# Kernel optimization log

Measured on AMD Instinct MI355X. Metric: run time of the kernel, lower is better.

Reference implementation:

```python
import jax, jax.numpy as jnp
import numpy as np

T, B, D, H = 512, 64, 1024, 1024


def _lstm_layer(x, W_ih, W_hh, b):
    """x: [T,B,in] -> (out [T,B,H], h_n [B,H], c_n [B,H]). Gate order i,f,g,o."""
    xW = jnp.einsum('tbi,ij->tbj', x, W_ih) + b  # precompute input projections [T,B,4H]
    Bsz = x.shape[1]
    Hsz = W_hh.shape[0]
    h0 = jnp.zeros((Bsz, Hsz), dtype=x.dtype)

    def step(carry, xw_t):
        h, c = carry
        gates = xw_t + h @ W_hh  # [B,4H]
        i, f, g, o = jnp.split(gates, 4, axis=-1)
        i = jax.nn.sigmoid(i)
        f = jax.nn.sigmoid(f)
        g = jnp.tanh(g)
        o = jax.nn.sigmoid(o)
        c_next = f * c + i * g
        h_next = o * jnp.tanh(c_next)
        return (h_next, c_next), h_next

    (h_n, c_n), out = jax.lax.scan(step, (h0, h0), xW)
    return out, h_n, c_n


def setup_inputs() -> dict:
    key = jax.random.key(0)
    ks = jax.random.split(key, 7)
    s_in = 1.0 / np.sqrt(H)
    return {
        'x': jax.random.normal(ks[0], (T, B, D), dtype=jnp.float32),
        'W_ih0': jax.random.normal(ks[1], (D, 4 * H), dtype=jnp.float32) * s_in,
        'W_hh0': jax.random.normal(ks[2], (H, 4 * H), dtype=jnp.float32) * s_in,
        'b0': jax.random.normal(ks[3], (4 * H,), dtype=jnp.float32) * s_in,
        'W_ih1': jax.random.normal(ks[4], (H, 4 * H), dtype=jnp.float32) * s_in,
        'W_hh1': jax.random.normal(ks[5], (H, 4 * H), dtype=jnp.float32) * s_in,
        'b1': jax.random.normal(ks[6], (4 * H,), dtype=jnp.float32) * s_in,
    }


def reference(x, W_ih0, W_hh0, b0, W_ih1, W_hh1, b1):
    # layer 0
    out0, h0n, c0n = _lstm_layer(x, W_ih0, W_hh0, b0)
    # dropout=0 -> identity between layers
    out1, h1n, c1n = _lstm_layer(out0, W_ih1, W_hh1, b1)
    h_n = jnp.stack([h0n, h1n], 0)  # [L,B,H]
    c_n = jnp.stack([c0n, c1n], 0)
    return out1, (h_n, c_n)
```

## Files before the change

kernel.cpp:

```cpp
#include <hip/hip_runtime.h>
#include <hip/hip_bf16.h>

#define TSTEPS 512
#define NSTEPS 256
#define BATCH  64
#define HDIM   1024
#define NROWS  (TSTEPS*BATCH)

typedef __attribute__((ext_vector_type(8))) short bf16x8;
typedef __attribute__((ext_vector_type(4))) float f32x4;

__device__ __forceinline__ unsigned short f2bf(float f){
    unsigned u = __float_as_uint(f);
    u += 0x7fffu + ((u >> 16) & 1u);
    return (unsigned short)(u >> 16);
}
__device__ __forceinline__ float bf2f(unsigned short s){
    return __uint_as_float(((unsigned)s) << 16);
}

__device__ __forceinline__ void gridbar(unsigned int* region, unsigned int epoch){
    unsigned int* slots = region;
    unsigned int* rel   = region + 8192;
    __syncthreads();
    if (blockIdx.x == 0){
        const int i = threadIdx.x;
        if (i > 0 && i < 256){
            while (__hip_atomic_load(&slots[i*32], __ATOMIC_RELAXED, __HIP_MEMORY_SCOPE_AGENT) < epoch)
                __builtin_amdgcn_s_sleep(2);
        }
        __syncthreads();
        if (i < 256){
            unsigned int old = __hip_atomic_exchange(&rel[i*32], epoch,
                                   __ATOMIC_RELAXED, __HIP_MEMORY_SCOPE_AGENT);
            asm volatile("" :: "v"(old));
        }
    } else {
        if (threadIdx.x == 0){
            unsigned int old = __hip_atomic_exchange(&slots[blockIdx.x*32], epoch,
                                   __ATOMIC_RELAXED, __HIP_MEMORY_SCOPE_AGENT);
            asm volatile("" :: "v"(old));
            while (__hip_atomic_load(&rel[blockIdx.x*32], __ATOMIC_RELAXED, __HIP_MEMORY_SCOPE_AGENT) < epoch)
                __builtin_amdgcn_s_sleep(2);
        }
        __syncthreads();
    }
    asm volatile("" ::: "memory");
}

__global__ __launch_bounds__(256)
void split_transpose_w(const float* __restrict__ W,
                       unsigned short* __restrict__ WThi,
                       unsigned short* __restrict__ WTlo)
{
    __shared__ float tile[32][33];
    const int c0 = blockIdx.x * 32;
    const int k0 = blockIdx.y * 32;
    const int tx = threadIdx.x & 31, ty = threadIdx.x >> 5;
    #pragma unroll
    for (int r=0;r<4;++r)
        tile[ty + r*8][tx] = W[(size_t)(k0 + ty + r*8)*4096 + c0 + tx];
    __syncthreads();
    #pragma unroll
    for (int r=0;r<4;++r){
        float v = tile[tx][ty + r*8];
        unsigned short hi = f2bf(v);
        unsigned short lo = f2bf(v - bf2f(hi));
        WThi[(size_t)(c0 + ty + r*8)*1024 + k0 + tx] = hi;
        WTlo[(size_t)(c0 + ty + r*8)*1024 + k0 + tx] = lo;
    }
}

__global__ __launch_bounds__(256)
void reorder_whh_t(const float* __restrict__ W,
                   unsigned short* __restrict__ Whi,
                   unsigned short* __restrict__ Wlo)
{
    const int bid = blockIdx.x;
    const int j  = threadIdx.x & 15;
    const int k0 = threadIdx.x >> 4;
    const int col = (j>>2)*1024 + bid*4 + (j&3);
    for (int k = k0; k < 1024; k += 16){
        float v = W[(size_t)k*4096 + col];
        unsigned short hi = f2bf(v);
        unsigned short lo = f2bf(v - bf2f(hi));
        Whi[((size_t)bid*16 + j)*1024 + k] = hi;
        Wlo[((size_t)bid*16 + j)*1024 + k] = lo;
    }
}

__global__ __launch_bounds__(256)
void gemm_xw_split(const float* __restrict__ A,
                   const unsigned short* __restrict__ BThi,
                   const unsigned short* __restrict__ BTlo,
                   const float* __restrict__ bias, unsigned short* __restrict__ gp)
{
    __shared__ __align__(16) unsigned short Ahi[128*32];
    __shared__ __align__(16) unsigned short Alo[128*32];
    __shared__ __align__(16) unsigned short Bhi[128*32];
    __shared__ __align__(16) unsigned short Blo[128*32];

    const int tid = threadIdx.x;
    const int w = tid >> 6, l = tid & 63;
    const int bx = blockIdx.x & 31, by = blockIdx.x >> 5;
    const int row0 = by*128, col0 = bx*128;
    const int wrow = (w>>1)*64, wcol = (w&1)*64;

    const int srow  = l >> 2;
    const int skoff = (l & 3) * 8;

    const int arow  = tid >> 1;
    const int akoff = (tid & 1) * 16;
    const float* aptr = A + (size_t)(row0 + arow)*1024 + akoff;

    f32x4 acc[4][4];
    #pragma unroll
    for (int m=0;m<4;++m)
        #pragma unroll
        for (int n=0;n<4;++n)
            acc[m][n] = (f32x4){0.f,0.f,0.f,0.f};

    for (int k0=0; k0<1024; k0+=32){
        #pragma unroll
        for (int c=0;c<2;++c){
            const int i = w*2 + c;
            const unsigned short* gh = BThi + (size_t)(col0 + i*16 + srow)*1024 + k0 + skoff;
            const unsigned short* gl = BTlo + (size_t)(col0 + i*16 + srow)*1024 + k0 + skoff;
            __builtin_amdgcn_global_load_lds((const __attribute__((address_space(1))) void*)gh,
                (__attribute__((address_space(3))) void*)(Bhi + i*512), 16, 0, 0);
            __builtin_amdgcn_global_load_lds((const __attribute__((address_space(1))) void*)gl,
                (__attribute__((address_space(3))) void*)(Blo + i*512), 16, 0, 0);
        }
        {
            float4 x0 = *reinterpret_cast<const float4*>(aptr + k0);
            float4 x1 = *reinterpret_cast<const float4*>(aptr + k0 + 4);
            float4 x2 = *reinterpret_cast<const float4*>(aptr + k0 + 8);
            float4 x3 = *reinterpret_cast<const float4*>(aptr + k0 + 12);
            float xs[16] = {x0.x,x0.y,x0.z,x0.w, x1.x,x1.y,x1.z,x1.w,
                            x2.x,x2.y,x2.z,x2.w, x3.x,x3.y,x3.z,x3.w};
            unsigned short hs[16], ls[16];
            #pragma unroll
            for (int e=0;e<16;++e){
                hs[e] = f2bf(xs[e]);
                ls[e] = f2bf(xs[e] - bf2f(hs[e]));
            }
            #pragma unroll
            for (int q=0;q<4;++q){
                ushort4 h4; h4.x=hs[q*4]; h4.y=hs[q*4+1]; h4.z=hs[q*4+2]; h4.w=hs[q*4+3];
                ushort4 l4; l4.x=ls[q*4]; l4.y=ls[q*4+1]; l4.z=ls[q*4+2]; l4.w=ls[q*4+3];
                *reinterpret_cast<ushort4*>(&Ahi[arow*32 + akoff + q*4]) = h4;
                *reinterpret_cast<ushort4*>(&Alo[arow*32 + akoff + q*4]) = l4;
            }
        }
        __syncthreads();
        bf16x8 afh[4], afl[4], bfh[4], bfl[4];
        #pragma unroll
        for (int m=0;m<4;++m){
            const int off = (wrow + m*16 + (l&15))*32 + (l>>4)*8;
            afh[m] = *reinterpret_cast<const bf16x8*>(&Ahi[off]);
            afl[m] = *reinterpret_cast<const bf16x8*>(&Alo[off]);
        }
        #pragma unroll
        for (int n=0;n<4;++n){
            const int off = (wcol + n*16 + (l&15))*32 + (l>>4)*8;
            bfh[n] = *reinterpret_cast<const bf16x8*>(&Bhi[off]);
            bfl[n] = *reinterpret_cast<const bf16x8*>(&Blo[off]);
        }
        #pragma unroll
        for (int m=0;m<4;++m)
            #pragma unroll
            for (int n=0;n<4;++n){
                acc[m][n] = __builtin_amdgcn_mfma_f32_16x16x32_bf16(afh[m], bfh[n], acc[m][n], 0,0,0);
                acc[m][n] = __builtin_amdgcn_mfma_f32_16x16x32_bf16(afl[m], bfh[n], acc[m][n], 0,0,0);
                acc[m][n] = __builtin_amdgcn_mfma_f32_16x16x32_bf16(afh[m], bfl[n], acc[m][n], 0,0,0);
            }
        __syncthreads();
    }

    #pragma unroll
    for (int n=0;n<4;++n){
        const int n_g = col0 + wcol + n*16 + (l&15);
        const float bv = bias[n_g];
        const int g = n_g >> 10, hcol = n_g & 1023;
        const int bid = hcol >> 2, hj = hcol & 3;
        #pragma unroll
        for (int m=0;m<4;++m){
            #pragma unroll
            for (int r=0;r<4;++r){
                const int m_g = row0 + wrow + m*16 + (l>>4)*4 + r;
                const int t = m_g >> 6, b = m_g & 63;
                gp[(((size_t)t*256 + bid)*64 + b)*16 + g*4 + hj] = f2bf(acc[m][n][r] + bv);
            }
        }
    }
}

__global__ __launch_bounds__(512)
void lstm_mfma(const unsigned short* __restrict__ gp,
               const unsigned short* __restrict__ Whi,
               const unsigned short* __restrict__ Wlo,
               float* __restrict__ out,
               unsigned short* __restrict__ rhi, unsigned short* __restrict__ rlo,
               float* __restrict__ ctg, float* __restrict__ hn, float* __restrict__ cn,
               unsigned int* __restrict__ bar, int first, int last)
{
    __shared__ float pacc[8][64*17];
    __shared__ float xwlds[64*17];
    __shared__ float hout[256];

    const int tid  = threadIdx.x;
    const int bidx = blockIdx.x;
    const int w = tid >> 6, l = tid & 63;
    const int kbase = w << 7;

    bf16x8 wfh[4], wfl[4];
    {
        const unsigned short* bh = Whi + ((size_t)bidx*16 + (l&15))*1024 + kbase + (l>>4)*8;
        const unsigned short* bl = Wlo + ((size_t)bidx*16 + (l&15))*1024 + kbase + (l>>4)*8;
        #pragma unroll
        for (int ks=0; ks<4; ++ks){
            wfh[ks] = *reinterpret_cast<const bf16x8*>(bh + ks*32);
            wfl[ks] = *reinterpret_cast<const bf16x8*>(bl + ks*32);
        }
    }

    float creg = 0.f;
    if (!first && tid < 256) creg = ctg[bidx*256 + tid];
    if (first && tid < 64){
        unsigned long long o1 = __hip_atomic_exchange(
            reinterpret_cast<unsigned long long*>(rhi + (size_t)256*65536 + tid*1024 + bidx*4),
            0ull, __ATOMIC_RELAXED, __HIP_MEMORY_SCOPE_AGENT);
        unsigned long long o2 = __hip_atomic_exchange(
            reinterpret_cast<unsigned long long*>(rlo + (size_t)256*65536 + tid*1024 + bidx*4),
            0ull, __ATOMIC_RELAXED, __HIP_MEMORY_SCOPE_AGENT);
        asm volatile("" :: "v"(o1), "v"(o2));
    }
    gridbar(bar, 1);

    const int bq = tid & 63;
    const int hc = tid >> 6;

    for (int t=0; t<NSTEPS; ++t){
        if (tid < 128){
            bf16x8 v = *reinterpret_cast<const bf16x8*>(
                gp + (size_t)t*262144 + (size_t)bidx*1024 + tid*8);
            const int b = tid >> 1, j0 = (tid & 1)*8;
            float* xp = &xwlds[b*17 + j0];
            #pragma unroll
            for (int e=0;e<8;++e) xp[e] = bf2f((unsigned short)v[e]);
        }

        const int rs = (t > 0) ? (t-1) : (first ? 256 : NSTEPS-1);
        const unsigned short* hbh = rhi + (size_t)rs*65536 + kbase + (l>>4)*8;
        const unsigned short* hbl = rlo + (size_t)rs*65536 + kbase + (l>>4)*8;

        f32x4 acc[4];
        #pragma unroll
        for (int mt=0; mt<4; ++mt) acc[mt] = (f32x4){0.f,0.f,0.f,0.f};

        #pragma unroll
        for (int mt=0; mt<4; ++mt){
            const size_t row = (size_t)(mt*16 + (l&15)) * 1024;
            #pragma unroll
            for (int ks=0; ks<4; ++ks){
                bf16x8 ah = *reinterpret_cast<const bf16x8*>(hbh + row + ks*32);
                bf16x8 al = *reinterpret_cast<const bf16x8*>(hbl + row + ks*32);
                acc[mt] = __builtin_amdgcn_mfma_f32_16x16x32_bf16(ah, wfh[ks], acc[mt], 0,0,0);
                acc[mt] = __builtin_amdgcn_mfma_f32_16x16x32_bf16(al, wfh[ks], acc[mt], 0,0,0);
                acc[mt] = __builtin_amdgcn_mfma_f32_16x16x32_bf16(ah, wfl[ks], acc[mt], 0,0,0);
            }
        }
        #pragma unroll
        for (int mt=0; mt<4; ++mt){
            #pragma unroll
            for (int r=0; r<4; ++r){
                const int m = mt*16 + (l>>4)*4 + r;
                pacc[w][m*17 + (l&15)] = acc[mt][r];
            }
        }
        __syncthreads();

        if (tid < 256){
            float gs[4];
            #pragma unroll
            for (int g=0; g<4; ++g){
                const int idx = bq*17 + g*4 + hc;
                float s = xwlds[idx];
                #pragma unroll
                for (int pw=0; pw<8; ++pw) s += pacc[pw][idx];
                gs[g] = s;
            }
            float ig = 1.f/(1.f + __expf(-gs[0]));
            float fg = 1.f/(1.f + __expf(-gs[1]));
            float gg = tanhf(gs[2]);
            float og = 1.f/(1.f + __expf(-gs[3]));
            float c_new = fg * creg + ig * gg;
            float h_new = og * tanhf(c_new);
            creg = c_new;
            hout[bq*4 + hc] = h_new;
            if (last && t == NSTEPS-1){
                const int hcolg = bidx*4 + hc;
                hn[(size_t)bq*1024 + hcolg] = h_new;
                cn[(size_t)bq*1024 + hcolg] = c_new;
            }
        }
        __syncthreads();

        if (tid < 64){
            const int b = tid;
            float h0 = hout[b*4+0], h1 = hout[b*4+1], h2 = hout[b*4+2], h3 = hout[b*4+3];
            unsigned short p0 = f2bf(h0), p1 = f2bf(h1), p2 = f2bf(h2), p3 = f2bf(h3);
            unsigned short q0 = f2bf(h0 - bf2f(p0)), q1 = f2bf(h1 - bf2f(p1));
            unsigned short q2 = f2bf(h2 - bf2f(p2)), q3 = f2bf(h3 - bf2f(p3));
            unsigned long long phi = (unsigned long long)p0 | ((unsigned long long)p1<<16)
                                   | ((unsigned long long)p2<<32) | ((unsigned long long)p3<<48);
            unsigned long long plo = (unsigned long long)q0 | ((unsigned long long)q1<<16)
                                   | ((unsigned long long)q2<<32) | ((unsigned long long)q3<<48);
            unsigned long long o1 = __hip_atomic_exchange(
                reinterpret_cast<unsigned long long*>(rhi + (size_t)t*65536 + b*1024 + bidx*4),
                phi, __ATOMIC_RELAXED, __HIP_MEMORY_SCOPE_AGENT);
            unsigned long long o2 = __hip_atomic_exchange(
                reinterpret_cast<unsigned long long*>(rlo + (size_t)t*65536 + b*1024 + bidx*4),
                plo, __ATOMIC_RELAXED, __HIP_MEMORY_SCOPE_AGENT);
            asm volatile("" :: "v"(o1), "v"(o2));
            *reinterpret_cast<float4*>(&out[(size_t)t*65536 + (size_t)b*1024 + bidx*4]) =
                make_float4(h0, h1, h2, h3);
        }
        gridbar(bar, t + 2);
    }
    if (tid < 256) ctg[bidx*256 + tid] = creg;
}

extern "C" void kernel_launch(void* const* d_in, const int* in_sizes, int n_in,
                              void* d_out, int out_size, void* d_ws, size_t ws_size,
                              hipStream_t stream)
{
    const float* x    = (const float*)d_in[0];
    const float* Wih0 = (const float*)d_in[1];
    const float* Whh0 = (const float*)d_in[2];
    const float* b0   = (const float*)d_in[3];
    const float* Wih1 = (const float*)d_in[4];
    const float* Whh1 = (const float*)d_in[5];
    const float* b1   = (const float*)d_in[6];

    float* out1 = (float*)d_out;
    float* hn   = out1 + (size_t)NROWS*HDIM;
    float* cn   = hn + 2*BATCH*HDIM;

    float* out0 = out1;

    char* wsb = (char*)d_ws;
    unsigned short* gp    = (unsigned short*)wsb;
    unsigned short* WThi0 = (unsigned short*)(wsb + 134217728ull);
    unsigned short* WTlo0 = (unsigned short*)(wsb + 142606336ull);
    unsigned short* WThi1 = (unsigned short*)(wsb + 150994944ull);
    unsigned short* WTlo1 = (unsigned short*)(wsb + 159383552ull);
    unsigned short* Wthi0 = (unsigned short*)(wsb + 167772160ull);
    unsigned short* Wtlo0 = (unsigned short*)(wsb + 176160768ull);
    unsigned short* Wthi1 = (unsigned short*)(wsb + 184549376ull);
    unsigned short* Wtlo1 = (unsigned short*)(wsb + 192937984ull);
    unsigned short* rhi   = (unsigned short*)(wsb + 201326592ull);
    unsigned short* rlo   = (unsigned short*)(wsb + 235012096ull);
    float*          ctg   = (float*)(wsb + 268697600ull);
    unsigned int*   bar   = (unsigned int*)(wsb + 268959744ull);

    hipMemsetAsync(bar, 0, 262144, stream);
    split_transpose_w<<<dim3(128,32),256,0,stream>>>(Wih0, WThi0, WTlo0);
    split_transpose_w<<<dim3(128,32),256,0,stream>>>(Wih1, WThi1, WTlo1);
    reorder_whh_t<<<256,256,0,stream>>>(Whh0, Wthi0, Wtlo0);
    reorder_whh_t<<<256,256,0,stream>>>(Whh1, Wthi1, Wtlo1);

    const float*          Ain [2] = {x, out0};
    const unsigned short* Whi [2] = {WThi0, WThi1};
    const unsigned short* Wlo [2] = {WTlo0, WTlo1};
    const float*          bia [2] = {b0, b1};
    const unsigned short* wth [2] = {Wthi0, Wthi1};
    const unsigned short* wtl [2] = {Wtlo0, Wtlo1};
    float*                outp[2] = {out0, out1};

    for (int layer=0; layer<2; ++layer){
        float* hnL = hn + (size_t)layer*BATCH*HDIM;
        float* cnL = cn + (size_t)layer*BATCH*HDIM;
        for (int chunk=0; chunk<2; ++chunk){
            gemm_xw_split<<<4096,256,0,stream>>>(
                Ain[layer] + (size_t)chunk*NSTEPS*BATCH*HDIM,
                Whi[layer], Wlo[layer], bia[layer], gp);

            const unsigned short* gpc = gp;
            const unsigned short* wh = wth[layer];
            const unsigned short* wl = wtl[layer];
            float* op = outp[layer] + (size_t)chunk*NSTEPS*BATCH*HDIM;
            unsigned short* r1 = rhi; unsigned short* r2 = rlo;
            float* cg_ = ctg;
            unsigned int* br = bar + (size_t)(layer*2 + chunk)*16384;
            int first = (chunk == 0), last = (chunk == 1);
            void* args[12] = {(void*)&gpc, (void*)&wh, (void*)&wl, (void*)&op,
                              (void*)&r1, (void*)&r2, (void*)&cg_,
                              (void*)&hnL, (void*)&cnL,
                              (void*)&br, (void*)&first, (void*)&last};
            hipLaunchCooperativeKernel(reinterpret_cast<void*>(&lstm_mfma),
                                       dim3(256), dim3(512), args, 0, stream);
        }
    }
}
```

Measured before the change: 13.43 ms.

## Fuse both LSTM layers into one wavefront-pipelined cooperative kernel

Replaces the per-layer recurrent kernels with a single 1024-thread-per-block kernel. One half of each block runs layer 0 at step r while the other half runs layer 1 at step r-1. Layer 1's input projection is computed inside the recurrence from layer 0's freshly published hidden state, so the separate layer-1 input GEMM and the layer-0 output round-trip through global memory go away. The number of grid-wide barriers roughly halves. In exchange, each step doubles block size and register pressure, and the layer-1 half does twice the MFMA work per step. The time is split into four chunks of 128 steps for the layer-0 input projection buffer.

New measurement: 15.35 ms. 1.14x slower.

```diff
diff --git a/kernel.cpp b/kernel.cpp
--- a/kernel.cpp
+++ b/kernel.cpp
@@ -2,7 +2,7 @@
 #include <hip/hip_bf16.h>
 
 #define TSTEPS 512
-#define NSTEPS 256
+#define NSTEPS 128
 #define BATCH  64
 #define HDIM   1024
 #define NROWS  (TSTEPS*BATCH)
@@ -195,99 +195,151 @@
     }
 }
 
-__global__ __launch_bounds__(512)
-void lstm_mfma(const unsigned short* __restrict__ gp,
-               const unsigned short* __restrict__ Whi,
-               const unsigned short* __restrict__ Wlo,
-               float* __restrict__ out,
-               unsigned short* __restrict__ rhi, unsigned short* __restrict__ rlo,
-               float* __restrict__ ctg, float* __restrict__ hn, float* __restrict__ cn,
-               unsigned int* __restrict__ bar, int first, int last)
+__global__ __launch_bounds__(1024)
+void lstm_fused(const unsigned short* __restrict__ gp,
+                const unsigned short* __restrict__ Wh0h, const unsigned short* __restrict__ Wh0l,
+                const unsigned short* __restrict__ Wi1h, const unsigned short* __restrict__ Wi1l,
+                const unsigned short* __restrict__ Wh1h, const unsigned short* __restrict__ Wh1l,
+                const float* __restrict__ bias1, float* __restrict__ out1,
+                unsigned short* __restrict__ r0h, unsigned short* __restrict__ r0l,
+                unsigned short* __restrict__ r1h, unsigned short* __restrict__ r1l,
+                float* __restrict__ ctg, float* __restrict__ hn, float* __restrict__ cn,
+                unsigned int* __restrict__ bar, int first, int last)
 {
-    __shared__ float pacc[8][64*17];
+    __shared__ float pacc[2][8][64*17];
     __shared__ float xwlds[64*17];
-    __shared__ float hout[256];
+    __shared__ float hout[2][256];
 
     const int tid  = threadIdx.x;
+    const int vb   = tid >> 9;
+    const int vt   = tid & 511;
     const int bidx = blockIdx.x;
-    const int w = tid >> 6, l = tid & 63;
+    const int w = vt >> 6, l = vt & 63;
     const int kbase = w << 7;
-
-    bf16x8 wfh[4], wfl[4];
+    const int foff = kbase + (l>>4)*8;
+
+    bf16x8 wah[4], wal[4], wbh[4], wbl[4];
     {
-        const unsigned short* bh = Whi + ((size_t)bidx*16 + (l&15))*1024 + kbase + (l>>4)*8;
-        const unsigned short* bl = Wlo + ((size_t)bidx*16 + (l&15))*1024 + kbase + (l>>4)*8;
+        const size_t wo = ((size_t)bidx*16 + (l&15))*1024 + foff;
+        const unsigned short* pah = (vb==0 ? Wh0h : Wi1h) + wo;
+        const unsigned short* pal = (vb==0 ? Wh0l : Wi1l) + wo;
         #pragma unroll
         for (int ks=0; ks<4; ++ks){
-            wfh[ks] = *reinterpret_cast<const bf16x8*>(bh + ks*32);
-            wfl[ks] = *reinterpret_cast<const bf16x8*>(bl + ks*32);
-        }
+            wah[ks] = *reinterpret_cast<const bf16x8*>(pah + ks*32);
+            wal[ks] = *reinterpret_cast<const bf16x8*>(pal + ks*32);
+        }
+        if (vb == 1){
+            const unsigned short* pbh = Wh1h + wo;
+            const unsigned short* pbl = Wh1l + wo;
+            #pragma unroll
+            for (int ks=0; ks<4; ++ks){
+                wbh[ks] = *reinterpret_cast<const bf16x8*>(pbh + ks*32);
+                wbl[ks] = *reinterpret_cast<const bf16x8*>(pbl + ks*32);
+            }
+        }
+    }
+
+    float b1r[4] = {0.f,0.f,0.f,0.f};
+    if (vb == 1 && vt < 256){
+        const int col = bidx*4 + (vt>>6);
+        #pragma unroll
+        for (int g=0; g<4; ++g) b1r[g] = bias1[g*1024 + col];
     }
 
     float creg = 0.f;
-    if (!first && tid < 256) creg = ctg[bidx*256 + tid];
-    if (first && tid < 64){
+    if (!first && vt < 256) creg = ctg[vb*65536 + bidx*256 + vt];
+    if (first && vt < 64){
+        unsigned short* rh = (vb==0) ? r0h : r1h;
+        unsigned short* rl = (vb==0) ? r0l : r1l;
         unsigned long long o1 = __hip_atomic_exchange(
-            reinterpret_cast<unsigned long long*>(rhi + (size_t)256*65536 + tid*1024 + bidx*4),
+            reinterpret_cast<unsigned long long*>(rh + (size_t)NSTEPS*65536 + vt*1024 + bidx*4),
             0ull, __ATOMIC_RELAXED, __HIP_MEMORY_SCOPE_AGENT);
         unsigned long long o2 = __hip_atomic_exchange(
-            reinterpret_cast<unsigned long long*>(rlo + (size_t)256*65536 + tid*1024 + bidx*4),
+            reinterpret_cast<unsigned long long*>(rl + (size_t)NSTEPS*65536 + vt*1024 + bidx*4),
             0ull, __ATOMIC_RELAXED, __HIP_MEMORY_SCOPE_AGENT);
         asm volatile("" :: "v"(o1), "v"(o2));
     }
     gridbar(bar, 1);
 
-    const int bq = tid & 63;
-    const int hc = tid >> 6;
-
-    for (int t=0; t<NSTEPS; ++t){
-        if (tid < 128){
-            bf16x8 v = *reinterpret_cast<const bf16x8*>(
-                gp + (size_t)t*262144 + (size_t)bidx*1024 + tid*8);
-            const int b = tid >> 1, j0 = (tid & 1)*8;
-            float* xp = &xwlds[b*17 + j0];
-            #pragma unroll
-            for (int e=0;e<8;++e) xp[e] = bf2f((unsigned short)v[e]);
-        }
-
-        const int rs = (t > 0) ? (t-1) : (first ? 256 : NSTEPS-1);
-        const unsigned short* hbh = rhi + (size_t)rs*65536 + kbase + (l>>4)*8;
-        const unsigned short* hbl = rlo + (size_t)rs*65536 + kbase + (l>>4)*8;
-
-        f32x4 acc[4];
-        #pragma unroll
-        for (int mt=0; mt<4; ++mt) acc[mt] = (f32x4){0.f,0.f,0.f,0.f};
-
-        #pragma unroll
-        for (int mt=0; mt<4; ++mt){
-            const size_t row = (size_t)(mt*16 + (l&15)) * 1024;
-            #pragma unroll
-            for (int ks=0; ks<4; ++ks){
-                bf16x8 ah = *reinterpret_cast<const bf16x8*>(hbh + row + ks*32);
-                bf16x8 al = *reinterpret_cast<const bf16x8*>(hbl + row + ks*32);
-                acc[mt] = __builtin_amdgcn_mfma_f32_16x16x32_bf16(ah, wfh[ks], acc[mt], 0,0,0);
-                acc[mt] = __builtin_amdgcn_mfma_f32_16x16x32_bf16(al, wfh[ks], acc[mt], 0,0,0);
-                acc[mt] = __builtin_amdgcn_mfma_f32_16x16x32_bf16(ah, wfl[ks], acc[mt], 0,0,0);
-            }
-        }
-        #pragma unroll
-        for (int mt=0; mt<4; ++mt){
-            #pragma unroll
-            for (int r=0; r<4; ++r){
-                const int m = mt*16 + (l>>4)*4 + r;
-                pacc[w][m*17 + (l&15)] = acc[mt][r];
-            }
-        }
-        __syncthreads();
-
-        if (tid < 256){
+    const int bq = vt & 63;
+    const int hc = vt >> 6;
+
+    for (int r=0; r<=NSTEPS; ++r){
+        if (vb == 0 && r < NSTEPS){
+            if (vt < 128){
+                bf16x8 v = *reinterpret_cast<const bf16x8*>(
+                    gp + (size_t)r*262144 + (size_t)bidx*1024 + vt*8);
+                const int b = vt >> 1, j0 = (vt & 1)*8;
+                float* xp = &xwlds[b*17 + j0];
+                #pragma unroll
+                for (int e=0;e<8;++e) xp[e] = bf2f((unsigned short)v[e]);
+            }
+            const int rs0 = (r > 0) ? r-1 : (first ? NSTEPS : NSTEPS-1);
+            const unsigned short* hbh = r0h + (size_t)rs0*65536 + foff;
+            const unsigned short* hbl = r0l + (size_t)rs0*65536 + foff;
+            f32x4 acc[4];
+            #pragma unroll
+            for (int mt=0; mt<4; ++mt) acc[mt] = (f32x4){0.f,0.f,0.f,0.f};
+            #pragma unroll
+            for (int mt=0; mt<4; ++mt){
+                const size_t row = (size_t)(mt*16 + (l&15)) * 1024;
+                #pragma unroll
+                for (int ks=0; ks<4; ++ks){
+                    bf16x8 ah = *reinterpret_cast<const bf16x8*>(hbh + row + ks*32);
+                    bf16x8 al = *reinterpret_cast<const bf16x8*>(hbl + row + ks*32);
+                    acc[mt] = __builtin_amdgcn_mfma_f32_16x16x32_bf16(ah, wah[ks], acc[mt], 0,0,0);
+                    acc[mt] = __builtin_amdgcn_mfma_f32_16x16x32_bf16(al, wah[ks], acc[mt], 0,0,0);
+                    acc[mt] = __builtin_amdgcn_mfma_f32_16x16x32_bf16(ah, wal[ks], acc[mt], 0,0,0);
+                }
+            }
+            #pragma unroll
+            for (int mt=0; mt<4; ++mt)
+                #pragma unroll
+                for (int q=0; q<4; ++q)
+                    pacc[0][w][(mt*16 + (l>>4)*4 + q)*17 + (l&15)] = acc[mt][q];
+        } else if (vb == 1 && r >= 1){
+            const unsigned short* xbh = r0h + (size_t)(r-1)*65536 + foff;
+            const unsigned short* xbl = r0l + (size_t)(r-1)*65536 + foff;
+            const int rs1 = (r >= 2) ? r-2 : (first ? NSTEPS : NSTEPS-1);
+            const unsigned short* hbh = r1h + (size_t)rs1*65536 + foff;
+            const unsigned short* hbl = r1l + (size_t)rs1*65536 + foff;
+            f32x4 acc[4];
+            #pragma unroll
+            for (int mt=0; mt<4; ++mt) acc[mt] = (f32x4){0.f,0.f,0.f,0.f};
+            #pragma unroll
+            for (int mt=0; mt<4; ++mt){
+                const size_t row = (size_t)(mt*16 + (l&15)) * 1024;
+                #pragma unroll
+                for (int ks=0; ks<4; ++ks){
+                    bf16x8 xh = *reinterpret_cast<const bf16x8*>(xbh + row + ks*32);
+                    bf16x8 xl = *reinterpret_cast<const bf16x8*>(xbl + row + ks*32);
+                    acc[mt] = __builtin_amdgcn_mfma_f32_16x16x32_bf16(xh, wah[ks], acc[mt], 0,0,0);
+                    acc[mt] = __builtin_amdgcn_mfma_f32_16x16x32_bf16(xl, wah[ks], acc[mt], 0,0,0);
+                    acc[mt] = __builtin_amdgcn_mfma_f32_16x16x32_bf16(xh, wal[ks], acc[mt], 0,0,0);
+                    bf16x8 ah = *reinterpret_cast<const bf16x8*>(hbh + row + ks*32);
+                    bf16x8 al = *reinterpret_cast<const bf16x8*>(hbl + row + ks*32);
+                    acc[mt] = __builtin_amdgcn_mfma_f32_16x16x32_bf16(ah, wbh[ks], acc[mt], 0,0,0);
+                    acc[mt] = __builtin_amdgcn_mfma_f32_16x16x32_bf16(al, wbh[ks], acc[mt], 0,0,0);
+                    acc[mt] = __builtin_amdgcn_mfma_f32_16x16x32_bf16(ah, wbl[ks], acc[mt], 0,0,0);
+                }
+            }
+            #pragma unroll
+            for (int mt=0; mt<4; ++mt)
+                #pragma unroll
+                for (int q=0; q<4; ++q)
+                    pacc[1][w][(mt*16 + (l>>4)*4 + q)*17 + (l&15)] = acc[mt][q];
+        }
+        __syncthreads();
+
+        const bool act = (vb==0) ? (r < NSTEPS) : (r >= 1);
+        if (vt < 256 && act){
             float gs[4];
             #pragma unroll
             for (int g=0; g<4; ++g){
                 const int idx = bq*17 + g*4 + hc;
-                float s = xwlds[idx];
-                #pragma unroll
-                for (int pw=0; pw<8; ++pw) s += pacc[pw][idx];
+                float s = (vb==0) ? xwlds[idx] : b1r[g];
+                #pragma unroll
+                for (int pw=0; pw<8; ++pw) s += pacc[vb][pw][idx];
                 gs[g] = s;
             }
             float ig = 1.f/(1.f + __expf(-gs[0]));
@@ -297,38 +349,47 @@
             float c_new = fg * creg + ig * gg;
             float h_new = og * tanhf(c_new);
             creg = c_new;
-            hout[bq*4 + hc] = h_new;
-            if (last && t == NSTEPS-1){
-                const int hcolg = bidx*4 + hc;
+            hout[vb][bq*4 + hc] = h_new;
+            const int hcolg = bidx*4 + hc;
+            if (vb==0 && last && r == NSTEPS-1){
                 hn[(size_t)bq*1024 + hcolg] = h_new;
                 cn[(size_t)bq*1024 + hcolg] = c_new;
             }
-        }
-        __syncthreads();
-
-        if (tid < 64){
-            const int b = tid;
-            float h0 = hout[b*4+0], h1 = hout[b*4+1], h2 = hout[b*4+2], h3 = hout[b*4+3];
-            unsigned short p0 = f2bf(h0), p1 = f2bf(h1), p2 = f2bf(h2), p3 = f2bf(h3);
-            unsigned short q0 = f2bf(h0 - bf2f(p0)), q1 = f2bf(h1 - bf2f(p1));
-            unsigned short q2 = f2bf(h2 - bf2f(p2)), q3 = f2bf(h3 - bf2f(p3));
+            if (vb==1 && last && r == NSTEPS){
+                hn[65536 + (size_t)bq*1024 + hcolg] = h_new;
+                cn[65536 + (size_t)bq*1024 + hcolg] = c_new;
+            }
+        }
+        __syncthreads();
+
+        if (vt < 64 && act){
+            const int b = vt;
+            float h0v = hout[vb][b*4+0], h1v = hout[vb][b*4+1];
+            float h2v = hout[vb][b*4+2], h3v = hout[vb][b*4+3];
+            unsigned short p0 = f2bf(h0v), p1 = f2bf(h1v), p2 = f2bf(h2v), p3 = f2bf(h3v);
+            unsigned short q0 = f2bf(h0v - bf2f(p0)), q1 = f2bf(h1v - bf2f(p1));
+            unsigned short q2 = f2bf(h2v - bf2f(p2)), q3 = f2bf(h3v - bf2f(p3));
             unsigned long long phi = (unsigned long long)p0 | ((unsigned long long)p1<<16)
                                    | ((unsigned long long)p2<<32) | ((unsigned long long)p3<<48);
             unsigned long long plo = (unsigned long long)q0 | ((unsigned long long)q1<<16)
                                    | ((unsigned long long)q2<<32) | ((unsigned long long)q3<<48);
+            const int slot = (vb==0) ? r : r-1;
+            unsigned short* rh = (vb==0) ? r0h : r1h;
+            unsigned short* rl = (vb==0) ? r0l : r1l;
             unsigned long long o1 = __hip_atomic_exchange(
-                reinterpret_cast<unsigned long long*>(rhi + (size_t)t*65536 + b*1024 + bidx*4),
+                reinterpret_cast<unsigned long long*>(rh + (size_t)slot*65536 + b*1024 + bidx*4),
                 phi, __ATOMIC_RELAXED, __HIP_MEMORY_SCOPE_AGENT);
             unsigned long long o2 = __hip_atomic_exchange(
-                reinterpret_cast<unsigned long long*>(rlo + (size_t)t*65536 + b*1024 + bidx*4),
+                reinterpret_cast<unsigned long long*>(rl + (size_t)slot*65536 + b*1024 + bidx*4),
                 plo, __ATOMIC_RELAXED, __HIP_MEMORY_SCOPE_AGENT);
             asm volatile("" :: "v"(o1), "v"(o2));
-            *reinterpret_cast<float4*>(&out[(size_t)t*65536 + (size_t)b*1024 + bidx*4]) =
-                make_float4(h0, h1, h2, h3);
-        }
-        gridbar(bar, t + 2);
-    }
-    if (tid < 256) ctg[bidx*256 + tid] = creg;
+            if (vb == 1)
+                *reinterpret_cast<float4*>(&out1[(size_t)(r-1)*65536 + (size_t)b*1024 + bidx*4]) =
+                    make_float4(h0v, h1v, h2v, h3v);
+        }
+        gridbar(bar, r + 2);
+    }
+    if (vt < 256) ctg[vb*65536 + bidx*256 + vt] = creg;
 }
 
 extern "C" void kernel_launch(void* const* d_in, const int* in_sizes, int n_in,
@@ -347,59 +408,50 @@
     float* hn   = out1 + (size_t)NROWS*HDIM;
     float* cn   = hn + 2*BATCH*HDIM;
 
-    float* out0 = out1;
-
     char* wsb = (char*)d_ws;
     unsigned short* gp    = (unsigned short*)wsb;
-    unsigned short* WThi0 = (unsigned short*)(wsb + 134217728ull);
-    unsigned short* WTlo0 = (unsigned short*)(wsb + 142606336ull);
-    unsigned short* WThi1 = (unsigned short*)(wsb + 150994944ull);
-    unsigned short* WTlo1 = (unsigned short*)(wsb + 159383552ull);
-    unsigned short* Wthi0 = (unsigned short*)(wsb + 167772160ull);
-    unsigned short* Wtlo0 = (unsigned short*)(wsb + 176160768ull);
-    unsigned short* Wthi1 = (unsigned short*)(wsb + 184549376ull);
-    unsigned short* Wtlo1 = (unsigned short*)(wsb + 192937984ull);
-    unsigned short* rhi   = (unsigned short*)(wsb + 201326592ull);
-    unsigned short* rlo   = (unsigned short*)(wsb + 235012096ull);
-    float*          ctg   = (float*)(wsb + 268697600ull);
-    unsigned int*   bar   = (unsigned int*)(wsb + 268959744ull);
+    unsigned short* WThi0 = (unsigned short*)(wsb +  67108864ull);
+    unsigned short* WTlo0 = (unsigned short*)(wsb +  75497472ull);
+    unsigned short* Wh0h  = (unsigned short*)(wsb +  83886080ull);
+    unsigned short* Wh0l  = (unsigned short*)(wsb +  92274688ull);
+    unsigned short* Wi1h  = (unsigned short*)(wsb + 100663296ull);
+    unsigned short* Wi1l  = (unsigned short*)(wsb + 109051904ull);
+    unsigned short* Wh1h  = (unsigned short*)(wsb + 117440512ull);
+    unsigned short* Wh1l  = (unsigned short*)(wsb + 125829120ull);
+    unsigned short* r0h   = (unsigned short*)(wsb + 134217728ull);
+    unsigned short* r0l   = (unsigned short*)(wsb + 151126016ull);
+    unsigned short* r1h   = (unsigned short*)(wsb + 168034304ull);
+    unsigned short* r1l   = (unsigned short*)(wsb + 184942592ull);
+    float*          ctg   = (float*)(wsb + 201850880ull);
+    unsigned int*   bar   = (unsigned int*)(wsb + 202375168ull);
 
     hipMemsetAsync(bar, 0, 262144, stream);
     split_transpose_w<<<dim3(128,32),256,0,stream>>>(Wih0, WThi0, WTlo0);
-    split_transpose_w<<<dim3(128,32),256,0,stream>>>(Wih1, WThi1, WTlo1);
-    reorder_whh_t<<<256,256,0,stream>>>(Whh0, Wthi0, Wtlo0);
-    reorder_whh_t<<<256,256,0,stream>>>(Whh1, Wthi1, Wtlo1);
-
-    const float*          Ain [2] = {x, out0};
-    const unsigned short* Whi [2] = {WThi0, WThi1};
-    const unsigned short* Wlo [2] = {WTlo0, WTlo1};
-    const float*          bia [2] = {b0, b1};
-    const unsigned short* wth [2] = {Wthi0, Wthi1};
-    const unsigned short* wtl [2] = {Wtlo0, Wtlo1};
-    float*                outp[2] = {out0, out1};
-
-    for (int layer=0; layer<2; ++layer){
-        float* hnL = hn + (size_t)layer*BATCH*HDIM;
-        float* cnL = cn + (size_t)layer*BATCH*HDIM;
-        for (int chunk=0; chunk<2; ++chunk){
-            gemm_xw_split<<<4096,256,0,stream>>>(
-                Ain[layer] + (size_t)chunk*NSTEPS*BATCH*HDIM,
-                Whi[layer], Wlo[layer], bia[layer], gp);
-
-            const unsigned short* gpc = gp;
-            const unsigned short* wh = wth[layer];
-            const unsigned short* wl = wtl[layer];
-            float* op = outp[layer] + (size_t)chunk*NSTEPS*BATCH*HDIM;
-            unsigned short* r1 = rhi; unsigned short* r2 = rlo;
-            float* cg_ = ctg;
-            unsigned int* br = bar + (size_t)(layer*2 + chunk)*16384;
-            int first = (chunk == 0), last = (chunk == 1);
-            void* args[12] = {(void*)&gpc, (void*)&wh, (void*)&wl, (void*)&op,
-                              (void*)&r1, (void*)&r2, (void*)&cg_,
-                              (void*)&hnL, (void*)&cnL,
-                              (void*)&br, (void*)&first, (void*)&last};
-            hipLaunchCooperativeKernel(reinterpret_cast<void*>(&lstm_mfma),
-                                       dim3(256), dim3(512), args, 0, stream);
-        }
-    }
-}
+    reorder_whh_t<<<256,256,0,stream>>>(Whh0, Wh0h, Wh0l);
+    reorder_whh_t<<<256,256,0,stream>>>(Wih1, Wi1h, Wi1l);
+    reorder_whh_t<<<256,256,0,stream>>>(Whh1, Wh1h, Wh1l);
+
+    for (int chunk=0; chunk<4; ++chunk){
+        gemm_xw_split<<<2048,256,0,stream>>>(
+            x + (size_t)chunk*NSTEPS*BATCH*HDIM, WThi0, WTlo0, b0, gp);
+
+        const unsigned short* gpc = gp;
+        const unsigned short* a0 = Wh0h; const unsigned short* a1 = Wh0l;
+        const unsigned short* a2 = Wi1h; const unsigned short* a3 = Wi1l;
+        const unsigned short* a4 = Wh1h; const unsigned short* a5 = Wh1l;
+        const float* bb1 = b1;
+        float* op = out1 + (size_t)chunk*NSTEPS*BATCH*HDIM;
+        unsigned short* p0 = r0h; unsigned short* p1 = r0l;
+        unsigned short* p2 = r1h; unsigned short* p3 = r1l;
+        float* cg_ = ctg; float* h_ = hn; float* c_ = cn;
+        unsigned int* br = bar + (size_t)chunk*16384;
+        int first = (chunk == 0), last = (chunk == 3);
+        void* args[19] = {(void*)&gpc, (void*)&a0, (void*)&a1, (void*)&a2, (void*)&a3,
+                          (void*)&a4, (void*)&a5, (void*)&bb1, (void*)&op,
+                          (void*)&p0, (void*)&p1, (void*)&p2, (void*)&p3,
+                          (void*)&cg_, (void*)&h_, (void*)&c_,
+                          (void*)&br, (void*)&first, (void*)&last};
+        hipLaunchCooperativeKernel(reinterpret_cast<void*>(&lstm_fused),
+                                   dim3(256), dim3(1024), args, 0, stream);
+    }
+}
```
